# Kernel tuning notes

Measured on AMD Instinct MI355X. Metric: run time of the kernel, lower is better.

Reference implementation:

```python
import jax, jax.numpy as jnp
import numpy as np

N, E = 100000, 1600000
IN_C, HID_C, OUT_C = 128, 64, 40


def setup_inputs() -> dict:
    key = jax.random.key(0)
    ks = jax.random.split(key, 8)
    s = lambda fan_in: 1.0 / np.sqrt(fan_in)
    return {
        "x": jax.random.normal(ks[0], (N, IN_C), dtype=jnp.float32),
        "edge_index": jax.random.randint(ks[1], (2, E), 0, N, dtype=jnp.int64),
        # SAGEConv layer 1: lin_l (on aggregated neighbors, with bias) + lin_r (root, no bias)
        "W_l1": jax.random.uniform(ks[2], (IN_C, HID_C), jnp.float32, -s(IN_C), s(IN_C)),
        "b_l1": jnp.zeros((HID_C,), jnp.float32),
        "W_r1": jax.random.uniform(ks[3], (IN_C, HID_C), jnp.float32, -s(IN_C), s(IN_C)),
        # SAGEConv layer 2
        "W_l2": jax.random.uniform(ks[4], (HID_C, OUT_C), jnp.float32, -s(HID_C), s(HID_C)),
        "b_l2": jnp.zeros((OUT_C,), jnp.float32),
        "W_r2": jax.random.uniform(ks[5], (HID_C, OUT_C), jnp.float32, -s(HID_C), s(HID_C)),
    }


def _sage_conv(x, src, dst, W_l, b_l, W_r, n_nodes):
    # mean-aggregate neighbor features: scatter-add x[src] onto dst, divide by degree
    agg = jax.ops.segment_sum(x[src], dst, num_segments=n_nodes)  # [N, F]
    deg = jax.ops.segment_sum(jnp.ones((src.shape[0],), x.dtype), dst, num_segments=n_nodes)
    mean = agg / jnp.maximum(deg, 1.0)[:, None]
    return mean @ W_l + b_l + x @ W_r


def reference(x, edge_index, W_l1, b_l1, W_r1, W_l2, b_l2, W_r2):
    src, dst = edge_index[0], edge_index[1]  # messages flow src -> dst
    # eval mode: dropout is identity
    hid = _sage_conv(x, src, dst, W_l1, b_l1, W_r1, N)
    hid = jax.nn.relu(hid)
    out = _sage_conv(hid, src, dst, W_l2, b_l2, W_r2, N)
    return jax.nn.log_softmax(out, axis=1)
```

## Files before the change

### kernel.cpp

```cpp
#include <hip/hip_runtime.h>
#include <hip/hip_bf16.h>

#define N_NODES 100000
#define E_EDGES 1600000
#define IN_C 128
#define HID_C 64
#define OUT_C 40

#define NBUCK 196
#define BCAP 9216
#define B1_EPT 16
#define B1_CHUNK (256 * B1_EPT)
#define B1_GRID ((E_EDGES + B1_CHUNK - 1) / B1_CHUNK)
#define TILE_GRID ((N_NODES + 63) / 64)

typedef unsigned short ushort_t;
typedef unsigned int uint_t;
typedef unsigned char uchar_t;
typedef __attribute__((ext_vector_type(8))) short bf16x8;
typedef __attribute__((ext_vector_type(4))) float f32x4;
typedef __attribute__((ext_vector_type(2))) float f32x2;

__device__ __forceinline__ float bfu2f(ushort_t u) {
    return __uint_as_float(((uint_t)u) << 16);
}
__device__ __forceinline__ ushort_t f2bfu(float f) {
    uint_t u = __float_as_uint(f);
    return (ushort_t)((u + 0x7FFFu + ((u >> 16) & 1u)) >> 16);
}
__device__ __forceinline__ uchar_t f2fp8(float f) {
    int p = __builtin_amdgcn_cvt_pk_fp8_f32(f, f, 0, false);
    return (uchar_t)(p & 0xff);
}

#define ACC8(A, U)                                                   \
    do {                                                             \
        (A)[0] += __builtin_amdgcn_cvt_pk_f32_fp8((U).x, false);     \
        (A)[1] += __builtin_amdgcn_cvt_pk_f32_fp8((U).x, true);      \
        (A)[2] += __builtin_amdgcn_cvt_pk_f32_fp8((U).y, false);     \
        (A)[3] += __builtin_amdgcn_cvt_pk_f32_fp8((U).y, true);      \
    } while (0)

__global__ __launch_bounds__(256) void k_prep(const int* __restrict__ src, const int* __restrict__ dst,
                                              int* __restrict__ bcur, int* __restrict__ bucket,
                                              const float* __restrict__ Wl1, const float* __restrict__ Wr1,
                                              const float* __restrict__ Wl2, const float* __restrict__ Wr2,
                                              ushort_t* __restrict__ Wt1, ushort_t* __restrict__ Wt2) {
    __shared__ int cnt[NBUCK];
    __shared__ int base[NBUCK];
    const int t = threadIdx.x;

    if (blockIdx.x < B1_GRID) {
        const int e0 = blockIdx.x * B1_CHUNK;
        for (int i = t; i < NBUCK; i += 256) cnt[i] = 0;
        __syncthreads();

        int myp[B1_EPT];
        int myb[B1_EPT];
#pragma unroll
        for (int j = 0; j < B1_EPT; ++j) {
            int e = e0 + t + j * 256;
            if (e < E_EDGES) {
                int d = dst[e];
                myp[j] = src[e] | ((d & 511) << 17);
                myb[j] = d >> 9;
                atomicAdd(&cnt[myb[j]], 1);
            } else {
                myb[j] = -1;
            }
        }
        __syncthreads();
        for (int i = t; i < NBUCK; i += 256) {
            base[i] = atomicAdd(&bcur[i], cnt[i]);
            cnt[i] = 0;
        }
        __syncthreads();
#pragma unroll
        for (int j = 0; j < B1_EPT; ++j) {
            if (myb[j] >= 0) {
                int b = myb[j];
                int loc = atomicAdd(&cnt[b], 1);
                int pos = base[b] + loc;
                if (pos < BCAP) bucket[(size_t)b * BCAP + pos] = myp[j];
            }
        }
    } else {
        int i = (blockIdx.x - B1_GRID) * 256 + t;
        if (i < 128 * 128) {
            int n = i >> 7, k = i & 127;
            float v = (n < 64) ? Wl1[k * 64 + n] : Wr1[k * 64 + (n - 64)];
            Wt1[n * 128 + k] = f2bfu(v);
        }
        if (i < 80 * 64) {
            int n = i >> 6, k = i & 63;
            float v = (n < 40) ? Wl2[k * 40 + n] : Wr2[k * 40 + (n - 40)];
            Wt2[n * 64 + k] = f2bfu(v);
        }
    }
}

struct SmemCsr {
    int red[256];
    int hist[512];
    int sc[2][512];
    int cur[512];
    int csrbuf[BCAP];
};
struct SmemGemm1 {
    ushort_t xs[64 * 136];
    ushort_t wsm[128 * 136];
};
union SmemK2 {
    SmemCsr c;
    SmemGemm1 g;
};

__global__ __launch_bounds__(256) void k_csr_gemm1(const int* __restrict__ bucket, const int* __restrict__ bcur,
                                                   int* __restrict__ rowptr, int* __restrict__ csr,
                                                   const float* __restrict__ x, const ushort_t* __restrict__ Wt,
                                                   uchar_t* __restrict__ h1l, ushort_t* __restrict__ h1r) {
    __shared__ SmemK2 sm;
    const int t = threadIdx.x;

    if (blockIdx.x < NBUCK) {
        const int b = blockIdx.x;
        const int n0 = b << 9;
        const int nb = min(512, N_NODES - n0);
        const int sz = min(bcur[b], BCAP);
        const int* bdata = bucket + (size_t)b * BCAP;

        int v = (t < b) ? min(bcur[t], BCAP) : 0;
        sm.c.red[t] = v;
        __syncthreads();
        for (int off = 128; off > 0; off >>= 1) {
            if (t < off) sm.c.red[t] += sm.c.red[t + off];
            __syncthreads();
        }
        const int cbase = sm.c.red[0];

        for (int i = t; i < 512; i += 256) sm.c.hist[i] = 0;
        __syncthreads();
        for (int i = t; i < sz; i += 256) {
            int p = bdata[i];
            atomicAdd(&sm.c.hist[p >> 17], 1);
        }
        __syncthreads();
        for (int i = t; i < 512; i += 256) sm.c.sc[0][i] = sm.c.hist[i];
        __syncthreads();
        int pp = 0;
        for (int off = 1; off < 512; off <<= 1) {
            for (int i = t; i < 512; i += 256)
                sm.c.sc[1 - pp][i] = sm.c.sc[pp][i] + ((i >= off) ? sm.c.sc[pp][i - off] : 0);
            __syncthreads();
            pp ^= 1;
        }
        for (int i = t; i < 512; i += 256) {
            int exc = sm.c.sc[pp][i] - sm.c.hist[i];
            sm.c.cur[i] = exc;
            if (i < nb) rowptr[n0 + i] = cbase + exc;
        }
        __syncthreads();
        for (int i = t; i < sz; i += 256) {
            int p = bdata[i];
            int pos = atomicAdd(&sm.c.cur[p >> 17], 1);
            sm.c.csrbuf[pos] = p & 0x1FFFF;
        }
        __syncthreads();
        for (int i = t; i < sz; i += 256)
            csr[cbase + i] = sm.c.csrbuf[i];
        if (b == NBUCK - 1 && t == 0) rowptr[N_NODES] = cbase + sz;
    } else {
        const int row_base = (blockIdx.x - NBUCK) * 64;

        for (int i = t; i < 128 * 16; i += 256) {
            int n = i >> 4, seg = i & 15;
            uint4 v = *(const uint4*)(Wt + n * 128 + seg * 8);
            *(uint4*)(sm.g.wsm + n * 136 + seg * 8) = v;
        }
        for (int i = t; i < 64 * 32; i += 256) {
            int row = i >> 5, seg = i & 31;
            int gr = row_base + row;
            float4 v = make_float4(0.f, 0.f, 0.f, 0.f);
            if (gr < N_NODES) v = *(const float4*)(x + (size_t)gr * IN_C + seg * 4);
            ushort4 u;
            u.x = f2bfu(v.x); u.y = f2bfu(v.y); u.z = f2bfu(v.z); u.w = f2bfu(v.w);
            *(ushort4*)(sm.g.xs + row * 136 + seg * 4) = u;
        }
        __syncthreads();

        const int wv = t >> 6, lane = t & 63;
        const int m = lane & 15, quad = lane >> 4;
        const int m0 = wv * 16;

        bf16x8 a[4];
#pragma unroll
        for (int kk = 0; kk < 4; ++kk)
            a[kk] = *(const bf16x8*)(sm.g.xs + (m0 + m) * 136 + kk * 32 + quad * 8);

        f32x4 acc[8];
#pragma unroll
        for (int nt = 0; nt < 8; ++nt) acc[nt] = (f32x4){0.f, 0.f, 0.f, 0.f};

#pragma unroll
        for (int nt = 0; nt < 8; ++nt) {
#pragma unroll
            for (int kk = 0; kk < 4; ++kk) {
                bf16x8 b = *(const bf16x8*)(sm.g.wsm + (nt * 16 + m) * 136 + kk * 32 + quad * 8);
                acc[nt] = __builtin_amdgcn_mfma_f32_16x16x32_bf16(a[kk], b, acc[nt], 0, 0, 0);
            }
        }

        const int grow_base = row_base + m0 + quad * 4;
#pragma unroll
        for (int r = 0; r < 4; ++r) {
            int grow = grow_base + r;
            if (grow < N_NODES) {
#pragma unroll
                for (int nt = 0; nt < 4; ++nt)
                    h1l[(size_t)grow * HID_C + nt * 16 + m] = f2fp8(acc[nt][r]);
#pragma unroll
                for (int nt = 4; nt < 8; ++nt)
                    h1r[(size_t)grow * HID_C + (nt - 4) * 16 + m] = f2bfu(acc[nt][r]);
            }
        }
    }
}

__global__ __launch_bounds__(256) void k_agg1_gemm2(const int* __restrict__ rowptr, const int* __restrict__ csr,
                                                    const uchar_t* __restrict__ h1l, const ushort_t* __restrict__ h1r,
                                                    const float* __restrict__ b1, const ushort_t* __restrict__ Wt,
                                                    uchar_t* __restrict__ h2l, ushort_t* __restrict__ h2r) {
    __shared__ ushort_t hs[64 * 72];
    __shared__ ushort_t wsm[80 * 72];
    const int t = threadIdx.x;
    const int row_base = blockIdx.x * 64;
    const int wv = t >> 6, lane = t & 63;
    const int slot = lane >> 3;
    const int part = lane & 7;

    for (int i = t; i < 80 * 8; i += 256) {
        int n = i >> 3, seg = i & 7;
        uint4 v = *(const uint4*)(Wt + n * 64 + seg * 8);
        *(uint4*)(wsm + n * 72 + seg * 8) = v;
    }

    float4 bb0, bb1;
    if (slot == 0) {
        bb0 = *(const float4*)(b1 + part * 8);
        bb1 = *(const float4*)(b1 + part * 8 + 4);
    }

    const int row0 = row_base + wv * 16;
    int rpv = 0;
    if (lane < 17) rpv = rowptr[min(row0 + lane, N_NODES)];

    for (int r16 = 0; r16 < 16; ++r16) {
        int lrow = wv * 16 + r16;
        int row = row0 + r16;
        if (row < N_NODES) {
            int start = __shfl(rpv, r16);
            int end = __shfl(rpv, r16 + 1);
            f32x2 acc[4];
#pragma unroll
            for (int j = 0; j < 4; ++j) acc[j] = (f32x2){0.f, 0.f};

            int base = start;
            for (; base + 16 <= end; base += 16) {
                int s0 = __builtin_nontemporal_load(&csr[base + slot]);
                int s1 = __builtin_nontemporal_load(&csr[base + slot + 8]);
                uint2 u0 = *(const uint2*)(h1l + (s0 << 6) + part * 8);
                uint2 u1 = *(const uint2*)(h1l + (s1 << 6) + part * 8);
                ACC8(acc, u0);
                ACC8(acc, u1);
            }
            if (base + 8 <= end) {
                int s0 = __builtin_nontemporal_load(&csr[base + slot]);
                uint2 u0 = *(const uint2*)(h1l + (s0 << 6) + part * 8);
                ACC8(acc, u0);
                base += 8;
            }
            if (base < end) {
                int e = base + slot;
                int s = __builtin_nontemporal_load(&csr[min(e, end - 1)]);
                uint2 u = *(const uint2*)(h1l + (s << 6) + part * 8);
                if (e >= end) { u.x = 0u; u.y = 0u; }
                ACC8(acc, u);
            }
#pragma unroll
            for (int off = 8; off <= 32; off <<= 1) {
#pragma unroll
                for (int j = 0; j < 4; ++j) {
                    f32x2 tt;
                    tt.x = __shfl_xor(acc[j].x, off);
                    tt.y = __shfl_xor(acc[j].y, off);
                    acc[j] += tt;
                }
            }
            if (slot == 0) {
                float inv = __builtin_amdgcn_rcpf(fmaxf((float)(end - start), 1.0f));
                ushort_t rr[8];
                *(uint4*)rr = *(const uint4*)(h1r + (size_t)row * HID_C + part * 8);
                ushort_t o[8];
                o[0] = f2bfu(fmaxf(acc[0].x * inv + bfu2f(rr[0]) + bb0.x, 0.f));
                o[1] = f2bfu(fmaxf(acc[0].y * inv + bfu2f(rr[1]) + bb0.y, 0.f));
                o[2] = f2bfu(fmaxf(acc[1].x * inv + bfu2f(rr[2]) + bb0.z, 0.f));
                o[3] = f2bfu(fmaxf(acc[1].y * inv + bfu2f(rr[3]) + bb0.w, 0.f));
                o[4] = f2bfu(fmaxf(acc[2].x * inv + bfu2f(rr[4]) + bb1.x, 0.f));
                o[5] = f2bfu(fmaxf(acc[2].y * inv + bfu2f(rr[5]) + bb1.y, 0.f));
                o[6] = f2bfu(fmaxf(acc[3].x * inv + bfu2f(rr[6]) + bb1.z, 0.f));
                o[7] = f2bfu(fmaxf(acc[3].y * inv + bfu2f(rr[7]) + bb1.w, 0.f));
                *(uint4*)(hs + lrow * 72 + part * 8) = *(const uint4*)o;
            }
        } else if (slot == 0) {
            uint4 z = make_uint4(0u, 0u, 0u, 0u);
            *(uint4*)(hs + lrow * 72 + part * 8) = z;
        }
    }
    __syncthreads();

    const int m = lane & 15, quad = lane >> 4;
    const int m0 = wv * 16;

    bf16x8 a[2];
#pragma unroll
    for (int kk = 0; kk < 2; ++kk)
        a[kk] = *(const bf16x8*)(hs + (m0 + m) * 72 + kk * 32 + quad * 8);

    f32x4 acc[5];
#pragma unroll
    for (int nt = 0; nt < 5; ++nt) acc[nt] = (f32x4){0.f, 0.f, 0.f, 0.f};

#pragma unroll
    for (int nt = 0; nt < 5; ++nt) {
#pragma unroll
        for (int kk = 0; kk < 2; ++kk) {
            bf16x8 b = *(const bf16x8*)(wsm + (nt * 16 + m) * 72 + kk * 32 + quad * 8);
            acc[nt] = __builtin_amdgcn_mfma_f32_16x16x32_bf16(a[kk], b, acc[nt], 0, 0, 0);
        }
    }

    const int grow_base = row_base + m0 + quad * 4;
#pragma unroll
    for (int r = 0; r < 4; ++r) {
        int grow = grow_base + r;
        if (grow < N_NODES) {
#pragma unroll
            for (int nt = 0; nt < 5; ++nt) {
                int col = nt * 16 + m;
                float v = acc[nt][r];
                if (col < OUT_C) h2l[(size_t)grow * 40 + col] = f2fp8(v);
                else             h2r[(size_t)grow * OUT_C + (col - OUT_C)] = f2bfu(v);
            }
        }
    }
}

__global__ __launch_bounds__(256) void k_agg2(const int* __restrict__ rowptr, const int* __restrict__ csr,
                                              const uchar_t* __restrict__ h2l, const ushort_t* __restrict__ h2r,
                                              const float* __restrict__ b2, float* __restrict__ out) {
    int row = (blockIdx.x * 256 + threadIdx.x) >> 6;
    int lane = threadIdx.x & 63;
    if (row >= N_NODES) return;
    int2 rp = *(const int2*)(rowptr + row);
    int start = rp.x, end = rp.y;
    const int slot = lane >> 3;
    const int part = lane & 7;
    f32x2 acc[4];
#pragma unroll
    for (int j = 0; j < 4; ++j) acc[j] = (f32x2){0.f, 0.f};

    int base = start;
    for (; base + 16 <= end; base += 16) {
        int s0 = __builtin_nontemporal_load(&csr[base + slot]);
        int s1 = __builtin_nontemporal_load(&csr[base + slot + 8]);
        uint2 u0 = *(const uint2*)(h2l + s0 * 40 + part * 8);
        uint2 u1 = *(const uint2*)(h2l + s1 * 40 + part * 8);
        ACC8(acc, u0);
        ACC8(acc, u1);
    }
    if (base + 8 <= end) {
        int s0 = __builtin_nontemporal_load(&csr[base + slot]);
        uint2 u0 = *(const uint2*)(h2l + s0 * 40 + part * 8);
        ACC8(acc, u0);
        base += 8;
    }
    if (base < end) {
        int e = base + slot;
        int s = __builtin_nontemporal_load(&csr[min(e, end - 1)]);
        uint2 u = *(const uint2*)(h2l + s * 40 + part * 8);
        if (e >= end) { u.x = 0u; u.y = 0u; }
        ACC8(acc, u);
    }
#pragma unroll
    for (int off = 8; off <= 32; off <<= 1) {
#pragma unroll
        for (int j = 0; j < 4; ++j) {
            f32x2 tt;
            tt.x = __shfl_xor(acc[j].x, off);
            tt.y = __shfl_xor(acc[j].y, off);
            acc[j] += tt;
        }
    }

    const bool fin = (slot == 0) && (part < 5);
    float inv = __builtin_amdgcn_rcpf(fmaxf((float)(end - start), 1.0f));
    f32x2 v2[4];
    if (fin) {
        size_t bi = (size_t)row * OUT_C + part * 8;
        ushort_t rr[8];
        *(uint2*)&rr[0] = *(const uint2*)(h2r + bi);
        *(uint2*)&rr[4] = *(const uint2*)(h2r + bi + 4);
        float4 bb0 = *(const float4*)(b2 + part * 8);
        float4 bb1 = *(const float4*)(b2 + part * 8 + 4);
        v2[0] = (f32x2){acc[0].x * inv + bfu2f(rr[0]) + bb0.x, acc[0].y * inv + bfu2f(rr[1]) + bb0.y};
        v2[1] = (f32x2){acc[1].x * inv + bfu2f(rr[2]) + bb0.z, acc[1].y * inv + bfu2f(rr[3]) + bb0.w};
        v2[2] = (f32x2){acc[2].x * inv + bfu2f(rr[4]) + bb1.x, acc[2].y * inv + bfu2f(rr[5]) + bb1.y};
        v2[3] = (f32x2){acc[3].x * inv + bfu2f(rr[6]) + bb1.z, acc[3].y * inv + bfu2f(rr[7]) + bb1.w};
    } else {
#pragma unroll
        for (int j = 0; j < 4; ++j) v2[j] = (f32x2){-1e30f, -1e30f};
    }
    f32x2 m2;
    m2.x = fmaxf(fmaxf(v2[0].x, v2[1].x), fmaxf(v2[2].x, v2[3].x));
    m2.y = fmaxf(fmaxf(v2[0].y, v2[1].y), fmaxf(v2[2].y, v2[3].y));
    float pm = fmaxf(m2.x, m2.y);
#pragma unroll
    for (int off = 1; off <= 4; off <<= 1) pm = fmaxf(pm, __shfl_xor(pm, off));
    float es = 0.f;
#pragma unroll
    for (int j = 0; j < 4; ++j) {
        es += __expf(v2[j].x - pm);
        es += __expf(v2[j].y - pm);
    }
#pragma unroll
    for (int off = 1; off <= 4; off <<= 1) es += __shfl_xor(es, off);
    float ls = __logf(es);
    if (fin) {
        size_t bo = (size_t)row * OUT_C + part * 8;
        *(float4*)(out + bo) = make_float4(v2[0].x - pm - ls, v2[0].y - pm - ls,
                                           v2[1].x - pm - ls, v2[1].y - pm - ls);
        *(float4*)(out + bo + 4) = make_float4(v2[2].x - pm - ls, v2[2].y - pm - ls,
                                               v2[3].x - pm - ls, v2[3].y - pm - ls);
    }
}

extern "C" void kernel_launch(void* const* d_in, const int* in_sizes, int n_in,
                              void* d_out, int out_size, void* d_ws, size_t ws_size,
                              hipStream_t stream) {
    const float* x   = (const float*)d_in[0];
    const int*   ei  = (const int*)d_in[1];
    const float* Wl1 = (const float*)d_in[2];
    const float* b1  = (const float*)d_in[3];
    const float* Wr1 = (const float*)d_in[4];
    const float* Wl2 = (const float*)d_in[5];
    const float* b2  = (const float*)d_in[6];
    const float* Wr2 = (const float*)d_in[7];

    size_t u = 0;
    int*      bucket = (int*)d_ws;             u += (size_t)NBUCK * BCAP;
    int*      bcur   = (int*)d_ws + u;         u += NBUCK + 4;
    int*      rowptr = (int*)d_ws + u;         u += N_NODES + 1;
    int*      csr    = (int*)d_ws + u;         u += E_EDGES;
    u = (u + 3) & ~(size_t)3;
    ushort_t* Wt1    = (ushort_t*)((int*)d_ws + u); u += 128 * 128 / 2;
    ushort_t* Wt2    = (ushort_t*)((int*)d_ws + u); u += 80 * 64 / 2;
    uchar_t*  h1l    = (uchar_t*)((int*)d_ws + u);  u += (size_t)N_NODES * HID_C / 4;
    ushort_t* h1r    = (ushort_t*)((int*)d_ws + u); u += (size_t)N_NODES * HID_C / 2;
    uchar_t*  h2l    = (uchar_t*)((int*)d_ws + u);  u += (size_t)N_NODES * 10 + 16;
    ushort_t* h2r    = (ushort_t*)((int*)d_ws + u); u += (size_t)N_NODES * OUT_C / 2;
    if (ws_size < u * 4) return;

    hipMemsetAsync(bcur, 0, NBUCK * sizeof(int), stream);

    const int* src = ei;
    const int* dst = ei + E_EDGES;

    k_prep<<<B1_GRID + 64, 256, 0, stream>>>(src, dst, bcur, bucket, Wl1, Wr1, Wl2, Wr2, Wt1, Wt2);
    k_csr_gemm1<<<NBUCK + TILE_GRID, 256, 0, stream>>>(bucket, bcur, rowptr, csr, x, Wt1, h1l, h1r);
    k_agg1_gemm2<<<TILE_GRID, 256, 0, stream>>>(rowptr, csr, h1l, h1r, b1, Wt2, h2l, h2r);
    k_agg2<<<N_NODES / 4, 256, 0, stream>>>(rowptr, csr, h2l, h2r, b2, (float*)d_out);
}
```

Before: 280.5 us.

## Stage CSR indices in LDS, widen gather loads, pad h2l rows to 64 bytes

New measurement: 299.0 us. +6.6%, slower.

```diff
diff --git a/kernel.cpp b/kernel.cpp
--- a/kernel.cpp
+++ b/kernel.cpp
@@ -13,6 +13,7 @@
 #define B1_CHUNK (256 * B1_EPT)
 #define B1_GRID ((E_EDGES + B1_CHUNK - 1) / B1_CHUNK)
 #define TILE_GRID ((N_NODES + 63) / 64)
+#define ECAP 384
 
 typedef unsigned short ushort_t;
 typedef unsigned int uint_t;
@@ -39,6 +40,18 @@
         (A)[1] += __builtin_amdgcn_cvt_pk_f32_fp8((U).x, true);      \
         (A)[2] += __builtin_amdgcn_cvt_pk_f32_fp8((U).y, false);     \
         (A)[3] += __builtin_amdgcn_cvt_pk_f32_fp8((U).y, true);      \
+    } while (0)
+
+#define ACC16(A, U)                                                  \
+    do {                                                             \
+        (A)[0] += __builtin_amdgcn_cvt_pk_f32_fp8((U).x, false);     \
+        (A)[1] += __builtin_amdgcn_cvt_pk_f32_fp8((U).x, true);      \
+        (A)[2] += __builtin_amdgcn_cvt_pk_f32_fp8((U).y, false);     \
+        (A)[3] += __builtin_amdgcn_cvt_pk_f32_fp8((U).y, true);      \
+        (A)[4] += __builtin_amdgcn_cvt_pk_f32_fp8((U).z, false);     \
+        (A)[5] += __builtin_amdgcn_cvt_pk_f32_fp8((U).z, true);      \
+        (A)[6] += __builtin_amdgcn_cvt_pk_f32_fp8((U).w, false);     \
+        (A)[7] += __builtin_amdgcn_cvt_pk_f32_fp8((U).w, true);      \
     } while (0)
 
 __global__ __launch_bounds__(256) void k_prep(const int* __restrict__ src, const int* __restrict__ dst,
@@ -232,11 +245,12 @@
                                                     uchar_t* __restrict__ h2l, ushort_t* __restrict__ h2r) {
     __shared__ ushort_t hs[64 * 72];
     __shared__ ushort_t wsm[80 * 72];
+    __shared__ int ecache[4][ECAP];
     const int t = threadIdx.x;
     const int row_base = blockIdx.x * 64;
     const int wv = t >> 6, lane = t & 63;
-    const int slot = lane >> 3;
-    const int part = lane & 7;
+    const int slot16 = lane >> 2;
+    const int part4 = lane & 3;
 
     for (int i = t; i < 80 * 8; i += 256) {
         int n = i >> 3, seg = i & 7;
@@ -244,76 +258,102 @@
         *(uint4*)(wsm + n * 72 + seg * 8) = v;
     }
 
-    float4 bb0, bb1;
-    if (slot == 0) {
-        bb0 = *(const float4*)(b1 + part * 8);
-        bb1 = *(const float4*)(b1 + part * 8 + 4);
+    float bv[16];
+    if (lane < 4) {
+#pragma unroll
+        for (int q = 0; q < 4; ++q) {
+            float4 b4 = *(const float4*)(b1 + lane * 16 + q * 4);
+            bv[4 * q + 0] = b4.x; bv[4 * q + 1] = b4.y;
+            bv[4 * q + 2] = b4.z; bv[4 * q + 3] = b4.w;
+        }
     }
 
     const int row0 = row_base + wv * 16;
     int rpv = 0;
     if (lane < 17) rpv = rowptr[min(row0 + lane, N_NODES)];
+    const int seg_start = __shfl(rpv, 0);
+    const int seg_end = __shfl(rpv, 16);
+    const int seg_len = seg_end - seg_start;
+    const bool fits = (seg_len <= ECAP);
+    {
+        int ld = min(seg_len, ECAP);
+        for (int i = lane; i < ld; i += 64)
+            ecache[wv][i] = csr[seg_start + i];
+    }
 
     for (int r16 = 0; r16 < 16; ++r16) {
-        int lrow = wv * 16 + r16;
-        int row = row0 + r16;
-        if (row < N_NODES) {
-            int start = __shfl(rpv, r16);
-            int end = __shfl(rpv, r16 + 1);
-            f32x2 acc[4];
-#pragma unroll
-            for (int j = 0; j < 4; ++j) acc[j] = (f32x2){0.f, 0.f};
-
+        const int lrow = wv * 16 + r16;
+        const int row = row0 + r16;
+        if (row >= N_NODES) {
+            if (lane < 4) {
+                uint4 z = make_uint4(0u, 0u, 0u, 0u);
+                *(uint4*)(hs + lrow * 72 + lane * 16) = z;
+                *(uint4*)(hs + lrow * 72 + lane * 16 + 8) = z;
+            }
+            continue;
+        }
+        const int start = __shfl(rpv, r16);
+        const int end = __shfl(rpv, r16 + 1);
+
+        f32x2 acc[8];
+#pragma unroll
+        for (int j = 0; j < 8; ++j) acc[j] = (f32x2){0.f, 0.f};
+
+        if (fits) {
+            const int lo = start - seg_start, hi = end - seg_start;
+            int base = lo;
+            for (; base + 16 <= hi; base += 16) {
+                int s = ecache[wv][base + slot16];
+                uint4 u = *(const uint4*)(h1l + ((size_t)s << 6) + part4 * 16);
+                ACC16(acc, u);
+            }
+            if (base < hi) {
+                int e = base + slot16;
+                int s = ecache[wv][min(e, hi - 1)];
+                uint4 u = *(const uint4*)(h1l + ((size_t)s << 6) + part4 * 16);
+                if (e >= hi) { u.x = 0u; u.y = 0u; u.z = 0u; u.w = 0u; }
+                ACC16(acc, u);
+            }
+        } else {
             int base = start;
             for (; base + 16 <= end; base += 16) {
-                int s0 = __builtin_nontemporal_load(&csr[base + slot]);
-                int s1 = __builtin_nontemporal_load(&csr[base + slot + 8]);
-                uint2 u0 = *(const uint2*)(h1l + (s0 << 6) + part * 8);
-                uint2 u1 = *(const uint2*)(h1l + (s1 << 6) + part * 8);
-                ACC8(acc, u0);
-                ACC8(acc, u1);
-            }
-            if (base + 8 <= end) {
-                int s0 = __builtin_nontemporal_load(&csr[base + slot]);
-                uint2 u0 = *(const uint2*)(h1l + (s0 << 6) + part * 8);
-                ACC8(acc, u0);
-                base += 8;
+                int s = csr[base + slot16];
+                uint4 u = *(const uint4*)(h1l + ((size_t)s << 6) + part4 * 16);
+                ACC16(acc, u);
             }
             if (base < end) {
-                int e = base + slot;
-                int s = __builtin_nontemporal_load(&csr[min(e, end - 1)]);
-                uint2 u = *(const uint2*)(h1l + (s << 6) + part * 8);
-                if (e >= end) { u.x = 0u; u.y = 0u; }
-                ACC8(acc, u);
-            }
-#pragma unroll
-            for (int off = 8; off <= 32; off <<= 1) {
-#pragma unroll
-                for (int j = 0; j < 4; ++j) {
-                    f32x2 tt;
-                    tt.x = __shfl_xor(acc[j].x, off);
-                    tt.y = __shfl_xor(acc[j].y, off);
-                    acc[j] += tt;
-                }
-            }
-            if (slot == 0) {
-                float inv = __builtin_amdgcn_rcpf(fmaxf((float)(end - start), 1.0f));
-                ushort_t rr[8];
-                *(uint4*)rr = *(const uint4*)(h1r + (size_t)row * HID_C + part * 8);
-                ushort_t o[8];
-                o[0] = f2bfu(fmaxf(acc[0].x * inv + bfu2f(rr[0]) + bb0.x, 0.f));
-                o[1] = f2bfu(fmaxf(acc[0].y * inv + bfu2f(rr[1]) + bb0.y, 0.f));
-                o[2] = f2bfu(fmaxf(acc[1].x * inv + bfu2f(rr[2]) + bb0.z, 0.f));
-                o[3] = f2bfu(fmaxf(acc[1].y * inv + bfu2f(rr[3]) + bb0.w, 0.f));
-                o[4] = f2bfu(fmaxf(acc[2].x * inv + bfu2f(rr[4]) + bb1.x, 0.f));
-                o[5] = f2bfu(fmaxf(acc[2].y * inv + bfu2f(rr[5]) + bb1.y, 0.f));
-                o[6] = f2bfu(fmaxf(acc[3].x * inv + bfu2f(rr[6]) + bb1.z, 0.f));
-                o[7] = f2bfu(fmaxf(acc[3].y * inv + bfu2f(rr[7]) + bb1.w, 0.f));
-                *(uint4*)(hs + lrow * 72 + part * 8) = *(const uint4*)o;
-            }
-        } else if (slot == 0) {
-            uint4 z = make_uint4(0u, 0u, 0u, 0u);
-            *(uint4*)(hs + lrow * 72 + part * 8) = z;
+                int e = base + slot16;
+                int s = csr[min(e, end - 1)];
+                uint4 u = *(const uint4*)(h1l + ((size_t)s << 6) + part4 * 16);
+                if (e >= end) { u.x = 0u; u.y = 0u; u.z = 0u; u.w = 0u; }
+                ACC16(acc, u);
+            }
+        }
+
+#pragma unroll
+        for (int off = 4; off <= 32; off <<= 1) {
+#pragma unroll
+            for (int j = 0; j < 8; ++j) {
+                f32x2 tt;
+                tt.x = __shfl_xor(acc[j].x, off);
+                tt.y = __shfl_xor(acc[j].y, off);
+                acc[j] += tt;
+            }
+        }
+
+        if (lane < 4) {
+            float inv = __builtin_amdgcn_rcpf(fmaxf((float)(end - start), 1.0f));
+            ushort_t rr[16];
+            *(uint4*)&rr[0] = *(const uint4*)(h1r + (size_t)row * HID_C + lane * 16);
+            *(uint4*)&rr[8] = *(const uint4*)(h1r + (size_t)row * HID_C + lane * 16 + 8);
+            ushort_t o[16];
+#pragma unroll
+            for (int j = 0; j < 8; ++j) {
+                o[2 * j]     = f2bfu(fmaxf(acc[j].x * inv + bfu2f(rr[2 * j])     + bv[2 * j],     0.f));
+                o[2 * j + 1] = f2bfu(fmaxf(acc[j].y * inv + bfu2f(rr[2 * j + 1]) + bv[2 * j + 1], 0.f));
+            }
+            *(uint4*)(hs + lrow * 72 + lane * 16) = *(const uint4*)&o[0];
+            *(uint4*)(hs + lrow * 72 + lane * 16 + 8) = *(const uint4*)&o[8];
         }
     }
     __syncthreads();
@@ -348,7 +388,7 @@
             for (int nt = 0; nt < 5; ++nt) {
                 int col = nt * 16 + m;
                 float v = acc[nt][r];
-                if (col < OUT_C) h2l[(size_t)grow * 40 + col] = f2fp8(v);
+                if (col < OUT_C) h2l[(size_t)grow * 64 + col] = f2fp8(v);
                 else             h2r[(size_t)grow * OUT_C + (col - OUT_C)] = f2bfu(v);
             }
         }
@@ -371,23 +411,23 @@
 
     int base = start;
     for (; base + 16 <= end; base += 16) {
-        int s0 = __builtin_nontemporal_load(&csr[base + slot]);
-        int s1 = __builtin_nontemporal_load(&csr[base + slot + 8]);
-        uint2 u0 = *(const uint2*)(h2l + s0 * 40 + part * 8);
-        uint2 u1 = *(const uint2*)(h2l + s1 * 40 + part * 8);
+        int s0 = csr[base + slot];
+        int s1 = csr[base + slot + 8];
+        uint2 u0 = *(const uint2*)(h2l + ((size_t)s0 << 6) + part * 8);
+        uint2 u1 = *(const uint2*)(h2l + ((size_t)s1 << 6) + part * 8);
         ACC8(acc, u0);
         ACC8(acc, u1);
     }
     if (base + 8 <= end) {
-        int s0 = __builtin_nontemporal_load(&csr[base + slot]);
-        uint2 u0 = *(const uint2*)(h2l + s0 * 40 + part * 8);
+        int s0 = csr[base + slot];
+        uint2 u0 = *(const uint2*)(h2l + ((size_t)s0 << 6) + part * 8);
         ACC8(acc, u0);
         base += 8;
     }
     if (base < end) {
         int e = base + slot;
-        int s = __builtin_nontemporal_load(&csr[min(e, end - 1)]);
-        uint2 u = *(const uint2*)(h2l + s * 40 + part * 8);
+        int s = csr[min(e, end - 1)];
+        uint2 u = *(const uint2*)(h2l + ((size_t)s << 6) + part * 8);
         if (e >= end) { u.x = 0u; u.y = 0u; }
         ACC8(acc, u);
     }
@@ -466,7 +506,7 @@
     ushort_t* Wt2    = (ushort_t*)((int*)d_ws + u); u += 80 * 64 / 2;
     uchar_t*  h1l    = (uchar_t*)((int*)d_ws + u);  u += (size_t)N_NODES * HID_C / 4;
     ushort_t* h1r    = (ushort_t*)((int*)d_ws + u); u += (size_t)N_NODES * HID_C / 2;
-    uchar_t*  h2l    = (uchar_t*)((int*)d_ws + u);  u += (size_t)N_NODES * 10 + 16;
+    uchar_t*  h2l    = (uchar_t*)((int*)d_ws + u);  u += (size_t)N_NODES * 64 / 4;
     ushort_t* h2r    = (ushort_t*)((int*)d_ws + u); u += (size_t)N_NODES * OUT_C / 2;
     if (ws_size < u * 4) return;
 
```
